# Kernel optimization log

Hardware: AMD Instinct MI355X
Metric: run time of the kernel (lower is better)

Reference implementation:

```python
import jax, jax.numpy as jnp
import numpy as np

B, T, D, H = 4, 1024, 1024, 16
NUM_BUCKETS = 320
MAX_DIST = 800
LN_EPS = 1e-5


def _rel_bucket(T):
    # bidirectional T5-style relative position buckets
    ctx = jnp.arange(T)[:, None]
    mem = jnp.arange(T)[None, :]
    rel = mem - ctx  # (T, T)
    half = NUM_BUCKETS // 2  # 160
    bucket = (rel > 0).astype(jnp.int32) * half
    n = jnp.abs(rel)
    max_exact = half // 2  # 80
    is_small = n < max_exact
    n_f = jnp.maximum(n, 1).astype(jnp.float32)
    large = max_exact + (
        jnp.log(n_f / max_exact) / np.log(MAX_DIST / max_exact) * (half - max_exact)
    ).astype(jnp.int32)
    large = jnp.minimum(large, half - 1)
    return bucket + jnp.where(is_small, n, large)


def setup_inputs() -> dict:
    key = jax.random.key(0)
    ks = jax.random.split(key, 12)
    s = 0.02
    return {
        "x": jax.random.normal(ks[0], (B, T, D), jnp.float32),
        "ln_w": jnp.ones((D,), jnp.float32),
        "ln_b": jnp.zeros((D,), jnp.float32),
        "wq": jax.random.normal(ks[1], (D, D), jnp.float32) * s,
        "bq": jnp.zeros((D,), jnp.float32),
        "wk": jax.random.normal(ks[2], (D, D), jnp.float32) * s,
        "bk": jnp.zeros((D,), jnp.float32),
        "wv": jax.random.normal(ks[3], (D, D), jnp.float32) * s,
        "bv": jnp.zeros((D,), jnp.float32),
        "wo": jax.random.normal(ks[4], (D, D), jnp.float32) * s,
        "bo": jnp.zeros((D,), jnp.float32),
        "rel_emb": jax.random.normal(ks[5], (NUM_BUCKETS, H), jnp.float32) * s,
        "grep_w": jax.random.normal(ks[6], (8, D // H), jnp.float32) * s,
        "grep_b": jnp.zeros((8,), jnp.float32),
        "grep_a": jnp.ones((1, H, 1, 1), jnp.float32),
    }


def reference(x, ln_w, ln_b, wq, bq, wk, bk, wv, bv, wo, bo, rel_emb, grep_w, grep_b, grep_a):
    Bb, Tt, Dd = x.shape
    hd = Dd // H
    scaling = hd ** -0.5
    # pre-norm LayerNorm
    mu = jnp.mean(x, -1, keepdims=True)
    var = jnp.mean((x - mu) ** 2, -1, keepdims=True)
    h = (x - mu) / jnp.sqrt(var + LN_EPS) * ln_w + ln_b
    # projections (q pre-scaled as in fairseq/WavLM)
    q = (h @ wq.T + bq) * scaling
    k = h @ wk.T + bk
    v = h @ wv.T + bv
    q = q.reshape(Bb, Tt, H, hd).transpose(0, 2, 1, 3)  # (B,H,T,hd)
    k = k.reshape(Bb, Tt, H, hd).transpose(0, 2, 1, 3)
    v = v.reshape(Bb, Tt, H, hd).transpose(0, 2, 1, 3)
    # bucketed relative position bias: (H, T, T)
    buckets = _rel_bucket(Tt)
    pos_bias = rel_emb[buckets].transpose(2, 0, 1)
    # gru_rel_pos gating (per batch, head, query position)
    alpha = 32.0
    ql = q * (alpha / scaling)  # undo scaling, multiply by alpha
    g = jax.nn.sigmoid((ql @ grep_w.T + grep_b).reshape(Bb, H, Tt, 2, 4).sum(-1))
    gate_a, gate_b = g[..., 0:1], g[..., 1:2]  # (B,H,T,1)
    gate = gate_a * (gate_b * grep_a - 1.0) + 2.0
    # attention
    scores = jnp.einsum('bhtd,bhsd->bhts', q, k) + gate * pos_bias[None]
    attn = jax.nn.softmax(scores, axis=-1)
    out = jnp.einsum('bhts,bhsd->bhtd', attn, v).transpose(0, 2, 1, 3).reshape(Bb, Tt, Dd)
    # output projection, dropout (identity in eval), residual
    out = out @ wo.T + bo + x
    pos_bias_out = jnp.broadcast_to(pos_bias[None], (Bb, H, Tt, Tt)).reshape(Bb * H, Tt, Tt)
    return out, pos_bias_out
```

## Files before the change

kernel.cpp:

```cpp
#include <hip/hip_runtime.h>

typedef unsigned short u16;
typedef __attribute__((ext_vector_type(8))) short short8;
typedef __attribute__((ext_vector_type(4))) float floatx4;

#define MFMA16(a, b, c) __builtin_amdgcn_mfma_f32_16x16x32_bf16(a, b, c, 0, 0, 0)

__device__ __forceinline__ float bf2f(u16 u) {
  return __uint_as_float(((unsigned int)u) << 16);
}
__device__ __forceinline__ u16 f2bf(float f) {
  unsigned int u = __float_as_uint(f);
  unsigned int r = (u + 0x7fffu + ((u >> 16) & 1u)) >> 16;
  return (u16)r;
}
__device__ __forceinline__ void gl_lds16(const u16* g, u16* lds_wave_base) {
  __builtin_amdgcn_global_load_lds(
      (const __attribute__((address_space(1))) unsigned int*)g,
      (__attribute__((address_space(3))) unsigned int*)lds_wave_base, 16, 0, 0);
}

__global__ __launch_bounds__(256) void ln_kernel(
    const float* __restrict__ x, const float* __restrict__ w, const float* __restrict__ bb,
    u16* __restrict__ hb)
{
  int wid = threadIdx.x >> 6, lane = threadIdx.x & 63;
  int row = blockIdx.x * 4 + wid;
  const float* xr = x + row * 1024 + lane * 16;
  float xs[16];
#pragma unroll
  for (int i = 0; i < 4; i++) {
    float4 v = *(const float4*)(xr + i * 4);
    xs[i * 4 + 0] = v.x; xs[i * 4 + 1] = v.y; xs[i * 4 + 2] = v.z; xs[i * 4 + 3] = v.w;
  }
  float s = 0.f, ss = 0.f;
#pragma unroll
  for (int i = 0; i < 16; i++) { s += xs[i]; ss += xs[i] * xs[i]; }
#pragma unroll
  for (int m = 1; m < 64; m <<= 1) { s += __shfl_xor(s, m, 64); ss += __shfl_xor(ss, m, 64); }
  float mu = s * (1.0f / 1024.0f);
  float var = ss * (1.0f / 1024.0f) - mu * mu;
  float rstd = rsqrtf(var + 1e-5f);
  const float* wr = w + lane * 16;
  const float* br = bb + lane * 16;
  short8 o0, o1;
#pragma unroll
  for (int i = 0; i < 8; i++) {
    o0[i] = (short)f2bf((xs[i] - mu) * rstd * wr[i] + br[i]);
    o1[i] = (short)f2bf((xs[8 + i] - mu) * rstd * wr[8 + i] + br[8 + i]);
  }
  u16* hr = hb + row * 1024 + lane * 16;
  *(short8*)hr = o0;
  *(short8*)(hr + 8) = o1;
}

__global__ __launch_bounds__(256) void convw_kernel(
    const float* __restrict__ wq, const float* __restrict__ wk,
    const float* __restrict__ wv, const float* __restrict__ wo,
    u16* __restrict__ wb)
{
  int idx = (blockIdx.x * 256 + threadIdx.x) * 8;
  int seg = idx >> 20, off = idx & 1048575;
  const float* s = (seg == 0) ? wq : (seg == 1) ? wk : (seg == 2) ? wv : wo;
  float4 f0 = *(const float4*)(s + off);
  float4 f1 = *(const float4*)(s + off + 4);
  short8 o;
  o[0] = (short)f2bf(f0.x); o[1] = (short)f2bf(f0.y);
  o[2] = (short)f2bf(f0.z); o[3] = (short)f2bf(f0.w);
  o[4] = (short)f2bf(f1.x); o[5] = (short)f2bf(f1.y);
  o[6] = (short)f2bf(f1.z); o[7] = (short)f2bf(f1.w);
  *(short8*)&wb[idx] = o;
}

__global__ __launch_bounds__(256) void qkv_kernel(
    const u16* __restrict__ hb, const u16* __restrict__ wb,
    const float* __restrict__ bq, const float* __restrict__ bk, const float* __restrict__ bv,
    u16* __restrict__ qs, u16* __restrict__ kko, u16* __restrict__ vt)
{
  __shared__ u16 As[128 * 32];
  __shared__ u16 Bs[128 * 32];
  int tid = threadIdx.x;
  int wid = tid >> 6, lane = tid & 63;
  int wm = wid >> 1, wn = wid & 1;
  int l15 = lane & 15, quad = lane >> 4;
  int m0 = blockIdx.y * 128;
  int n0g = blockIdx.x * 128;
  int sec = n0g >> 10;
  int n0 = n0g & 1023;
  const u16* W = wb + sec * 1048576;
  const float* bias = (sec == 0) ? bq : ((sec == 1) ? bk : bv);

  floatx4 zero4 = {0.f, 0.f, 0.f, 0.f};
  floatx4 acc[4][4];
#pragma unroll
  for (int i = 0; i < 4; i++)
#pragma unroll
    for (int j = 0; j < 4; j++) acc[i][j] = zero4;

  int lr = tid >> 2;
  int lc = (tid & 3) * 8;
  u16* asw = As + wid * 512;
  u16* bsw = Bs + wid * 512;

  for (int kt = 0; kt < 1024; kt += 32) {
    gl_lds16(&hb[(m0 + lr) * 1024 + kt + lc],      asw);
    gl_lds16(&hb[(m0 + lr + 64) * 1024 + kt + lc], asw + 2048);
    gl_lds16(&W[(n0 + lr) * 1024 + kt + lc],       bsw);
    gl_lds16(&W[(n0 + lr + 64) * 1024 + kt + lc],  bsw + 2048);
    __syncthreads();
    short8 af[4], bf[4];
#pragma unroll
    for (int mi = 0; mi < 4; mi++)
      af[mi] = *(const short8*)&As[(wm * 64 + mi * 16 + l15) * 32 + quad * 8];
#pragma unroll
    for (int ni = 0; ni < 4; ni++)
      bf[ni] = *(const short8*)&Bs[(wn * 64 + ni * 16 + l15) * 32 + quad * 8];
#pragma unroll
    for (int mi = 0; mi < 4; mi++)
#pragma unroll
      for (int ni = 0; ni < 4; ni++)
        acc[mi][ni] = MFMA16(af[mi], bf[ni], acc[mi][ni]);
    __syncthreads();
  }

  int bidx = m0 >> 10;
#pragma unroll
  for (int mi = 0; mi < 4; mi++) {
#pragma unroll
    for (int ni = 0; ni < 4; ni++) {
#pragma unroll
      for (int r = 0; r < 4; r++) {
        int row = m0 + wm * 64 + mi * 16 + quad * 4 + r;
        int t = row & 1023;
        int c = n0 + wn * 64 + ni * 16 + l15;
        float val = acc[mi][ni][r] + bias[c];
        int hh = c >> 6, hp = c & 63;
        if (sec == 0) {
          val *= 0.125f;
          qs[((bidx * 16 + hh) * 1024 + t) * 64 + hp] = f2bf(val);
        } else if (sec == 1) {
          kko[((bidx * 16 + hh) * 1024 + t) * 64 + hp] = f2bf(val);
        } else {
          vt[((bidx * 16 + hh) * 64 + hp) * 1024 + t] = f2bf(val);
        }
      }
    }
  }
}

__device__ __forceinline__ int rel_bucket(int t, int s) {
  int rel = s - t;
  int bucket = (rel > 0) ? 160 : 0;
  int n = (rel < 0) ? -rel : rel;
  if (n < 80) return bucket + n;
  float a = logf((float)n / 80.0f);
  float c = a / (float)2.302585092994046;
  float v = c * 80.0f;
  int large = 80 + (int)v;
  if (large > 159) large = 159;
  return bucket + large;
}

__global__ __launch_bounds__(256) void bias0_kernel(
    const float* __restrict__ rel_emb, float* __restrict__ out1,
    u16* __restrict__ bh16, int nb4)
{
  int tid = blockIdx.x * 256 + threadIdx.x;
  int t = tid >> 7;
  int s0 = (tid & 127) * 8;
  int bkt[8];
#pragma unroll
  for (int j = 0; j < 8; j++) bkt[j] = rel_bucket(t, s0 + j) * 16;
  int base_ts = t * 1024 + s0;
#pragma unroll
  for (int hh = 0; hh < 16; hh++) {
    float4 v0, v1;
    v0.x = rel_emb[bkt[0] + hh]; v0.y = rel_emb[bkt[1] + hh];
    v0.z = rel_emb[bkt[2] + hh]; v0.w = rel_emb[bkt[3] + hh];
    v1.x = rel_emb[bkt[4] + hh]; v1.y = rel_emb[bkt[5] + hh];
    v1.z = rel_emb[bkt[6] + hh]; v1.w = rel_emb[bkt[7] + hh];
    float* p = out1 + hh * 1048576 + base_ts;
    *(float4*)p = v0;
    *(float4*)(p + 4) = v1;
    if (nb4) {
      *(float4*)(p + 16777216) = v0; *(float4*)(p + 16777216 + 4) = v1;
      *(float4*)(p + 33554432) = v0; *(float4*)(p + 33554432 + 4) = v1;
      *(float4*)(p + 50331648) = v0; *(float4*)(p + 50331648 + 4) = v1;
    }
    short8 o;
    o[0] = (short)f2bf(v0.x); o[1] = (short)f2bf(v0.y);
    o[2] = (short)f2bf(v0.z); o[3] = (short)f2bf(v0.w);
    o[4] = (short)f2bf(v1.x); o[5] = (short)f2bf(v1.y);
    o[6] = (short)f2bf(v1.z); o[7] = (short)f2bf(v1.w);
    *(short8*)(bh16 + hh * 1048576 + base_ts) = o;
  }
}

__global__ __launch_bounds__(256) void bias_copy_kernel(float* __restrict__ out1)
{
  int idx = blockIdx.x * 256 + threadIdx.x;
  float4 v = *(const float4*)&out1[idx * 4];
  *(float4*)&out1[16777216 + idx * 4] = v;
  *(float4*)&out1[33554432 + idx * 4] = v;
  *(float4*)&out1[50331648 + idx * 4] = v;
}

__global__ __launch_bounds__(256) void attn_kernel(
    const u16* __restrict__ qs, const u16* __restrict__ kko, const u16* __restrict__ vt,
    const float* __restrict__ gw, const float* __restrict__ gb, const float* __restrict__ ga,
    const u16* __restrict__ bh16, u16* __restrict__ ao)
{
  __shared__ __align__(16) u16 Pb[4][16 * 64];
  int wid = threadIdx.x >> 6, lane = threadIdx.x & 63;
  int l15 = lane & 15, quad = lane >> 4;
  int bh = blockIdx.x;
  int b = bh >> 4, h = bh & 15;
  int q0 = blockIdx.y * 64 + wid * 16;
  const u16* Q = qs + bh * 65536;
  const u16* K = kko + bh * 65536;
  const u16* V = vt + bh * 65536;
  const u16* Bi = bh16 + h * 1048576;
  u16* pb = &Pb[wid][0];

  const u16* qrow = Q + (q0 + l15) * 64;
  float e[8];
#pragma unroll
  for (int i = 0; i < 8; i++) e[i] = gb[i];
  for (int j = 0; j < 64; j++) {
    float ql = bf2f(qrow[j]) * 256.0f;
#pragma unroll
    for (int i = 0; i < 8; i++) e[i] += ql * gw[i * 64 + j];
  }
  float u0 = e[0] + e[1] + e[2] + e[3];
  float u1 = e[4] + e[5] + e[6] + e[7];
  float sa = 1.0f / (1.0f + __expf(-u0));
  float sb = 1.0f / (1.0f + __expf(-u1));
  float gv = sa * (sb * ga[h] - 1.0f) + 2.0f;

  short8 qf0 = *(const short8*)&Q[(q0 + l15) * 64 + quad * 8];
  short8 qf1 = *(const short8*)&Q[(q0 + l15) * 64 + quad * 8 + 32];
  float gt[4], mrun[4], lrun[4];
#pragma unroll
  for (int r = 0; r < 4; r++) {
    gt[r] = __shfl(gv, quad * 4 + r, 64);
    mrun[r] = -1e30f;
    lrun[r] = 0.f;
  }
  floatx4 zero4 = {0.f, 0.f, 0.f, 0.f};
  floatx4 accO[4];
#pragma unroll
  for (int ni = 0; ni < 4; ni++) accO[ni] = zero4;

  for (int s0 = 0; s0 < 1024; s0 += 64) {
    floatx4 sc[4];
#pragma unroll
    for (int j = 0; j < 4; j++) sc[j] = zero4;
    short8 kf;
#pragma unroll
    for (int j = 0; j < 4; j++) {
      kf = *(const short8*)&K[(s0 + j * 16 + l15) * 64 + quad * 8];
      sc[j] = MFMA16(qf0, kf, sc[j]);
      kf = *(const short8*)&K[(s0 + j * 16 + l15) * 64 + quad * 8 + 32];
      sc[j] = MFMA16(qf1, kf, sc[j]);
    }

#pragma unroll
    for (int r = 0; r < 4; r++) {
      int t = q0 + quad * 4 + r;
      float v[4];
#pragma unroll
      for (int j = 0; j < 4; j++)
        v[j] = sc[j][r] + gt[r] * bf2f(Bi[t * 1024 + s0 + j * 16 + l15]);
      float mt = fmaxf(fmaxf(v[0], v[1]), fmaxf(v[2], v[3]));
#pragma unroll
      for (int m = 1; m < 16; m <<= 1) mt = fmaxf(mt, __shfl_xor(mt, m, 64));
      float mnew = fmaxf(mrun[r], mt);
      float alpha = __expf(fmaxf(mrun[r] - mnew, -80.0f));
      float p[4], ps = 0.f;
#pragma unroll
      for (int j = 0; j < 4; j++) { p[j] = __expf(v[j] - mnew); ps += p[j]; }
#pragma unroll
      for (int m = 1; m < 16; m <<= 1) ps += __shfl_xor(ps, m, 64);
      lrun[r] = lrun[r] * alpha + ps;
      mrun[r] = mnew;
#pragma unroll
      for (int ni = 0; ni < 4; ni++) accO[ni][r] *= alpha;
#pragma unroll
      for (int j = 0; j < 4; j++)
        pb[(quad * 4 + r) * 64 + j * 16 + l15] = f2bf(p[j]);
    }
    __syncthreads();
    short8 pf0 = *(const short8*)&pb[l15 * 64 + quad * 8];
    short8 pf1 = *(const short8*)&pb[l15 * 64 + 32 + quad * 8];
#pragma unroll
    for (int ni = 0; ni < 4; ni++) {
      short8 vf = *(const short8*)&V[(ni * 16 + l15) * 1024 + s0 + quad * 8];
      accO[ni] = MFMA16(pf0, vf, accO[ni]);
      vf = *(const short8*)&V[(ni * 16 + l15) * 1024 + s0 + 32 + quad * 8];
      accO[ni] = MFMA16(pf1, vf, accO[ni]);
    }
  }
#pragma unroll
  for (int ni = 0; ni < 4; ni++) {
#pragma unroll
    for (int r = 0; r < 4; r++) {
      int t = q0 + quad * 4 + r;
      float val = accO[ni][r] / lrun[r];
      ao[(b * 1024 + t) * 1024 + h * 64 + ni * 16 + l15] = f2bf(val);
    }
  }
}

__global__ __launch_bounds__(256) void oproj_kernel(
    const u16* __restrict__ ao, const u16* __restrict__ wob, const float* __restrict__ bo,
    const float* __restrict__ x, float* __restrict__ out)
{
  __shared__ u16 As[128 * 32];
  __shared__ u16 Bs[128 * 32];
  int tid = threadIdx.x;
  int wid = tid >> 6, lane = tid & 63;
  int wm = wid >> 1, wn = wid & 1;
  int l15 = lane & 15, quad = lane >> 4;
  int m0 = blockIdx.y * 128;
  int n0 = blockIdx.x * 128;

  floatx4 zero4 = {0.f, 0.f, 0.f, 0.f};
  floatx4 acc[4][4];
#pragma unroll
  for (int i = 0; i < 4; i++)
#pragma unroll
    for (int j = 0; j < 4; j++) acc[i][j] = zero4;

  int lr = tid >> 2;
  int lc = (tid & 3) * 8;
  u16* asw = As + wid * 512;
  u16* bsw = Bs + wid * 512;

  for (int kt = 0; kt < 1024; kt += 32) {
    gl_lds16(&ao[(m0 + lr) * 1024 + kt + lc],       asw);
    gl_lds16(&ao[(m0 + lr + 64) * 1024 + kt + lc],  asw + 2048);
    gl_lds16(&wob[(n0 + lr) * 1024 + kt + lc],      bsw);
    gl_lds16(&wob[(n0 + lr + 64) * 1024 + kt + lc], bsw + 2048);
    __syncthreads();
    short8 af[4], bf[4];
#pragma unroll
    for (int mi = 0; mi < 4; mi++)
      af[mi] = *(const short8*)&As[(wm * 64 + mi * 16 + l15) * 32 + quad * 8];
#pragma unroll
    for (int ni = 0; ni < 4; ni++)
      bf[ni] = *(const short8*)&Bs[(wn * 64 + ni * 16 + l15) * 32 + quad * 8];
#pragma unroll
    for (int mi = 0; mi < 4; mi++)
#pragma unroll
      for (int ni = 0; ni < 4; ni++)
        acc[mi][ni] = MFMA16(af[mi], bf[ni], acc[mi][ni]);
    __syncthreads();
  }

#pragma unroll
  for (int mi = 0; mi < 4; mi++) {
#pragma unroll
    for (int ni = 0; ni < 4; ni++) {
#pragma unroll
      for (int r = 0; r < 4; r++) {
        int row = m0 + wm * 64 + mi * 16 + quad * 4 + r;
        int c = n0 + wn * 64 + ni * 16 + l15;
        out[row * 1024 + c] = acc[mi][ni][r] + bo[c] + x[row * 1024 + c];
      }
    }
  }
}

extern "C" void kernel_launch(void* const* d_in, const int* in_sizes, int n_in,
                              void* d_out, int out_size, void* d_ws, size_t ws_size,
                              hipStream_t stream) {
  const float* x    = (const float*)d_in[0];
  const float* ln_w = (const float*)d_in[1];
  const float* ln_b = (const float*)d_in[2];
  const float* wq   = (const float*)d_in[3];
  const float* bq   = (const float*)d_in[4];
  const float* wk   = (const float*)d_in[5];
  const float* bk   = (const float*)d_in[6];
  const float* wv   = (const float*)d_in[7];
  const float* bv   = (const float*)d_in[8];
  const float* wo   = (const float*)d_in[9];
  const float* bo   = (const float*)d_in[10];
  const float* rel  = (const float*)d_in[11];
  const float* gw   = (const float*)d_in[12];
  const float* gb   = (const float*)d_in[13];
  const float* ga   = (const float*)d_in[14];

  float* out0  = (float*)d_out;
  float* out1f = out0 + 4194304;

  int big_ws = (ws_size >= (size_t)(96u << 20)) ? 1 : 0;
  char* sb = big_ws ? (char*)d_ws : (char*)(out1f + 16777216);
  u16* hbb = (u16*)(sb);
  u16* wbb = (u16*)(sb + (8u << 20));
  u16* qsb = (u16*)(sb + (16u << 20));
  u16* kkb = (u16*)(sb + (24u << 20));
  u16* vtb = (u16*)(sb + (32u << 20));
  u16* aob = (u16*)(sb + (40u << 20));
  u16* bhb = (u16*)(sb + (48u << 20));

  ln_kernel<<<1024, 256, 0, stream>>>(x, ln_w, ln_b, hbb);
  convw_kernel<<<2048, 256, 0, stream>>>(wq, wk, wv, wo, wbb);
  qkv_kernel<<<dim3(24, 32), 256, 0, stream>>>(hbb, wbb, bq, bk, bv, qsb, kkb, vtb);
  bias0_kernel<<<512, 256, 0, stream>>>(rel, out1f, bhb, big_ws);
  attn_kernel<<<dim3(64, 16), 256, 0, stream>>>(qsb, kkb, vtb, gw, gb, ga, bhb, aob);
  oproj_kernel<<<dim3(8, 32), 256, 0, stream>>>(aob, wbb + 3145728, bo, x, out0);
  if (!big_ws)
    bias_copy_kernel<<<16384, 256, 0, stream>>>(out1f);
}
```

Measured before the change: 594.6 us.

## Defer softmax row-sum reduction, pad P LDS tile, replace barrier with waitcnt

In the attention kernel, each lane now keeps a per-lane partial row sum and does the cross-lane shuffle reduction once at the end, instead of reducing every 64-key tile. The block-wide __syncthreads before reading the P tile becomes an lgkmcnt wait, since each wave only reads its own LDS slice. The P tile rows are padded from 64 to 68 elements to cut LDS bank conflicts, and the bias loads are hoisted ahead of the QK MFMAs to overlap their latency. The risks are relying on intra-wave LDS ordering without a barrier and the padded layout forcing 8-byte LDS reads instead of 16-byte ones.

Measured after the change: 552.2 us. 1.08x faster.

```diff
diff --git a/kernel.cpp b/kernel.cpp
--- a/kernel.cpp
+++ b/kernel.cpp
@@ -2,6 +2,7 @@
 
 typedef unsigned short u16;
 typedef __attribute__((ext_vector_type(8))) short short8;
+typedef __attribute__((ext_vector_type(4))) short short4v;
 typedef __attribute__((ext_vector_type(4))) float floatx4;
 
 #define MFMA16(a, b, c) __builtin_amdgcn_mfma_f32_16x16x32_bf16(a, b, c, 0, 0, 0)
@@ -210,7 +211,7 @@
     const float* __restrict__ gw, const float* __restrict__ gb, const float* __restrict__ ga,
     const u16* __restrict__ bh16, u16* __restrict__ ao)
 {
-  __shared__ __align__(16) u16 Pb[4][16 * 64];
+  __shared__ __align__(16) u16 Pb[4][16 * 68];
   int wid = threadIdx.x >> 6, lane = threadIdx.x & 63;
   int l15 = lane & 15, quad = lane >> 4;
   int bh = blockIdx.x;
@@ -239,12 +240,12 @@
 
   short8 qf0 = *(const short8*)&Q[(q0 + l15) * 64 + quad * 8];
   short8 qf1 = *(const short8*)&Q[(q0 + l15) * 64 + quad * 8 + 32];
-  float gt[4], mrun[4], lrun[4];
+  float gt[4], mrun[4], lsum[4];
 #pragma unroll
   for (int r = 0; r < 4; r++) {
     gt[r] = __shfl(gv, quad * 4 + r, 64);
     mrun[r] = -1e30f;
-    lrun[r] = 0.f;
+    lsum[r] = 0.f;
   }
   floatx4 zero4 = {0.f, 0.f, 0.f, 0.f};
   floatx4 accO[4];
@@ -252,13 +253,20 @@
   for (int ni = 0; ni < 4; ni++) accO[ni] = zero4;
 
   for (int s0 = 0; s0 < 1024; s0 += 64) {
+    float bi[4][4];
+#pragma unroll
+    for (int r = 0; r < 4; r++) {
+      int t = q0 + quad * 4 + r;
+#pragma unroll
+      for (int j = 0; j < 4; j++)
+        bi[r][j] = bf2f(Bi[t * 1024 + s0 + j * 16 + l15]);
+    }
     floatx4 sc[4];
 #pragma unroll
     for (int j = 0; j < 4; j++) sc[j] = zero4;
-    short8 kf;
 #pragma unroll
     for (int j = 0; j < 4; j++) {
-      kf = *(const short8*)&K[(s0 + j * 16 + l15) * 64 + quad * 8];
+      short8 kf = *(const short8*)&K[(s0 + j * 16 + l15) * 64 + quad * 8];
       sc[j] = MFMA16(qf0, kf, sc[j]);
       kf = *(const short8*)&K[(s0 + j * 16 + l15) * 64 + quad * 8 + 32];
       sc[j] = MFMA16(qf1, kf, sc[j]);
@@ -266,32 +274,33 @@
 
 #pragma unroll
     for (int r = 0; r < 4; r++) {
-      int t = q0 + quad * 4 + r;
       float v[4];
 #pragma unroll
-      for (int j = 0; j < 4; j++)
-        v[j] = sc[j][r] + gt[r] * bf2f(Bi[t * 1024 + s0 + j * 16 + l15]);
+      for (int j = 0; j < 4; j++) v[j] = sc[j][r] + gt[r] * bi[r][j];
       float mt = fmaxf(fmaxf(v[0], v[1]), fmaxf(v[2], v[3]));
 #pragma unroll
       for (int m = 1; m < 16; m <<= 1) mt = fmaxf(mt, __shfl_xor(mt, m, 64));
       float mnew = fmaxf(mrun[r], mt);
       float alpha = __expf(fmaxf(mrun[r] - mnew, -80.0f));
-      float p[4], ps = 0.f;
-#pragma unroll
-      for (int j = 0; j < 4; j++) { p[j] = __expf(v[j] - mnew); ps += p[j]; }
-#pragma unroll
-      for (int m = 1; m < 16; m <<= 1) ps += __shfl_xor(ps, m, 64);
-      lrun[r] = lrun[r] * alpha + ps;
+      float p[4];
+#pragma unroll
+      for (int j = 0; j < 4; j++) p[j] = __expf(v[j] - mnew);
+      lsum[r] = lsum[r] * alpha + (p[0] + p[1]) + (p[2] + p[3]);
       mrun[r] = mnew;
 #pragma unroll
       for (int ni = 0; ni < 4; ni++) accO[ni][r] *= alpha;
 #pragma unroll
       for (int j = 0; j < 4; j++)
-        pb[(quad * 4 + r) * 64 + j * 16 + l15] = f2bf(p[j]);
-    }
-    __syncthreads();
-    short8 pf0 = *(const short8*)&pb[l15 * 64 + quad * 8];
-    short8 pf1 = *(const short8*)&pb[l15 * 64 + 32 + quad * 8];
+        pb[(quad * 4 + r) * 68 + j * 16 + l15] = f2bf(p[j]);
+    }
+    __asm__ __volatile__("s_waitcnt lgkmcnt(0)" ::: "memory");
+    short4v a0 = *(const short4v*)&pb[l15 * 68 + quad * 8];
+    short4v a1 = *(const short4v*)&pb[l15 * 68 + quad * 8 + 4];
+    short4v a2 = *(const short4v*)&pb[l15 * 68 + 32 + quad * 8];
+    short4v a3 = *(const short4v*)&pb[l15 * 68 + 32 + quad * 8 + 4];
+    short8 pf0, pf1;
+#pragma unroll
+    for (int i = 0; i < 4; i++) { pf0[i] = a0[i]; pf0[4 + i] = a1[i]; pf1[i] = a2[i]; pf1[4 + i] = a3[i]; }
 #pragma unroll
     for (int ni = 0; ni < 4; ni++) {
       short8 vf = *(const short8*)&V[(ni * 16 + l15) * 1024 + s0 + quad * 8];
@@ -300,13 +309,20 @@
       accO[ni] = MFMA16(pf1, vf, accO[ni]);
     }
   }
+  float linv[4];
+#pragma unroll
+  for (int r = 0; r < 4; r++) {
+    float ls = lsum[r];
+#pragma unroll
+    for (int m = 1; m < 16; m <<= 1) ls += __shfl_xor(ls, m, 64);
+    linv[r] = 1.0f / ls;
+  }
 #pragma unroll
   for (int ni = 0; ni < 4; ni++) {
 #pragma unroll
     for (int r = 0; r < 4; r++) {
       int t = q0 + quad * 4 + r;
-      float val = accO[ni][r] / lrun[r];
-      ao[(b * 1024 + t) * 1024 + h * 64 + ni * 16 + l15] = f2bf(val);
+      ao[(b * 1024 + t) * 1024 + h * 64 + ni * 16 + l15] = f2bf(accO[ni][r] * linv[r]);
     }
   }
 }
```

## Transpose attention score tiles so each lane owns one query column

Applied to the files above, without the earlier changes.

Swaps the MFMA operands so that score and output tiles are computed transposed. Each lane now holds one query's scores, which lets the softmax max and sum be reduced mostly in registers with two cross-quad shuffles instead of per-row 16-lane shuffle trees. The bf16 bias table is written transposed so the attention kernel's bias reads become contiguous across lanes. It also pads the P buffer in LDS, replaces `__syncthreads` with a wave-local `lgkmcnt` wait, adds an occupancy hint to the launch bounds, and stages the final output through LDS to restore row-major stores. In exchange it adds extra LDS round trips and relies on the P buffer being private to each wave.

Result: faster. 567.7 us (-4.5%).

```diff
diff --git a/kernel.cpp b/kernel.cpp
--- a/kernel.cpp
+++ b/kernel.cpp
@@ -2,6 +2,7 @@
 
 typedef unsigned short u16;
 typedef __attribute__((ext_vector_type(8))) short short8;
+typedef __attribute__((ext_vector_type(4))) short short4v;
 typedef __attribute__((ext_vector_type(4))) float floatx4;
 
 #define MFMA16(a, b, c) __builtin_amdgcn_mfma_f32_16x16x32_bf16(a, b, c, 0, 0, 0)
@@ -168,9 +169,12 @@
   int tid = blockIdx.x * 256 + threadIdx.x;
   int t = tid >> 7;
   int s0 = (tid & 127) * 8;
-  int bkt[8];
-#pragma unroll
-  for (int j = 0; j < 8; j++) bkt[j] = rel_bucket(t, s0 + j) * 16;
+  int bkt[8], bktT[8];
+#pragma unroll
+  for (int j = 0; j < 8; j++) {
+    bkt[j]  = rel_bucket(t, s0 + j) * 16;
+    bktT[j] = rel_bucket(s0 + j, t) * 16;
+  }
   int base_ts = t * 1024 + s0;
 #pragma unroll
   for (int hh = 0; hh < 16; hh++) {
@@ -188,10 +192,8 @@
       *(float4*)(p + 50331648) = v0; *(float4*)(p + 50331648 + 4) = v1;
     }
     short8 o;
-    o[0] = (short)f2bf(v0.x); o[1] = (short)f2bf(v0.y);
-    o[2] = (short)f2bf(v0.z); o[3] = (short)f2bf(v0.w);
-    o[4] = (short)f2bf(v1.x); o[5] = (short)f2bf(v1.y);
-    o[6] = (short)f2bf(v1.z); o[7] = (short)f2bf(v1.w);
+#pragma unroll
+    for (int j = 0; j < 8; j++) o[j] = (short)f2bf(rel_emb[bktT[j] + hh]);
     *(short8*)(bh16 + hh * 1048576 + base_ts) = o;
   }
 }
@@ -205,12 +207,12 @@
   *(float4*)&out1[50331648 + idx * 4] = v;
 }
 
-__global__ __launch_bounds__(256) void attn_kernel(
+__global__ __launch_bounds__(256, 4) void attn_kernel(
     const u16* __restrict__ qs, const u16* __restrict__ kko, const u16* __restrict__ vt,
     const float* __restrict__ gw, const float* __restrict__ gb, const float* __restrict__ ga,
     const u16* __restrict__ bh16, u16* __restrict__ ao)
 {
-  __shared__ __align__(16) u16 Pb[4][16 * 64];
+  __shared__ __align__(16) u16 Pb[4][16 * 72];
   int wid = threadIdx.x >> 6, lane = threadIdx.x & 63;
   int l15 = lane & 15, quad = lane >> 4;
   int bh = blockIdx.x;
@@ -219,7 +221,7 @@
   const u16* Q = qs + bh * 65536;
   const u16* K = kko + bh * 65536;
   const u16* V = vt + bh * 65536;
-  const u16* Bi = bh16 + h * 1048576;
+  const u16* BiT = bh16 + h * 1048576;
   u16* pb = &Pb[wid][0];
 
   const u16* qrow = Q + (q0 + l15) * 64;
@@ -235,17 +237,11 @@
   float u1 = e[4] + e[5] + e[6] + e[7];
   float sa = 1.0f / (1.0f + __expf(-u0));
   float sb = 1.0f / (1.0f + __expf(-u1));
-  float gv = sa * (sb * ga[h] - 1.0f) + 2.0f;
+  float gt = sa * (sb * ga[h] - 1.0f) + 2.0f;
 
   short8 qf0 = *(const short8*)&Q[(q0 + l15) * 64 + quad * 8];
   short8 qf1 = *(const short8*)&Q[(q0 + l15) * 64 + quad * 8 + 32];
-  float gt[4], mrun[4], lrun[4];
-#pragma unroll
-  for (int r = 0; r < 4; r++) {
-    gt[r] = __shfl(gv, quad * 4 + r, 64);
-    mrun[r] = -1e30f;
-    lrun[r] = 0.f;
-  }
+  float mrun = -1e30f, lsum = 0.f;
   floatx4 zero4 = {0.f, 0.f, 0.f, 0.f};
   floatx4 accO[4];
 #pragma unroll
@@ -254,59 +250,70 @@
   for (int s0 = 0; s0 < 1024; s0 += 64) {
     floatx4 sc[4];
 #pragma unroll
-    for (int j = 0; j < 4; j++) sc[j] = zero4;
-    short8 kf;
-#pragma unroll
-    for (int j = 0; j < 4; j++) {
-      kf = *(const short8*)&K[(s0 + j * 16 + l15) * 64 + quad * 8];
-      sc[j] = MFMA16(qf0, kf, sc[j]);
-      kf = *(const short8*)&K[(s0 + j * 16 + l15) * 64 + quad * 8 + 32];
-      sc[j] = MFMA16(qf1, kf, sc[j]);
-    }
-
-#pragma unroll
-    for (int r = 0; r < 4; r++) {
-      int t = q0 + quad * 4 + r;
-      float v[4];
-#pragma unroll
-      for (int j = 0; j < 4; j++)
-        v[j] = sc[j][r] + gt[r] * bf2f(Bi[t * 1024 + s0 + j * 16 + l15]);
-      float mt = fmaxf(fmaxf(v[0], v[1]), fmaxf(v[2], v[3]));
-#pragma unroll
-      for (int m = 1; m < 16; m <<= 1) mt = fmaxf(mt, __shfl_xor(mt, m, 64));
-      float mnew = fmaxf(mrun[r], mt);
-      float alpha = __expf(fmaxf(mrun[r] - mnew, -80.0f));
-      float p[4], ps = 0.f;
-#pragma unroll
-      for (int j = 0; j < 4; j++) { p[j] = __expf(v[j] - mnew); ps += p[j]; }
-#pragma unroll
-      for (int m = 1; m < 16; m <<= 1) ps += __shfl_xor(ps, m, 64);
-      lrun[r] = lrun[r] * alpha + ps;
-      mrun[r] = mnew;
-#pragma unroll
-      for (int ni = 0; ni < 4; ni++) accO[ni][r] *= alpha;
-#pragma unroll
-      for (int j = 0; j < 4; j++)
-        pb[(quad * 4 + r) * 64 + j * 16 + l15] = f2bf(p[j]);
-    }
-    __syncthreads();
-    short8 pf0 = *(const short8*)&pb[l15 * 64 + quad * 8];
-    short8 pf1 = *(const short8*)&pb[l15 * 64 + 32 + quad * 8];
+    for (int tile = 0; tile < 4; tile++) {
+      short8 kf = *(const short8*)&K[(s0 + tile * 16 + l15) * 64 + quad * 8];
+      sc[tile] = MFMA16(kf, qf0, zero4);
+      kf = *(const short8*)&K[(s0 + tile * 16 + l15) * 64 + quad * 8 + 32];
+      sc[tile] = MFMA16(kf, qf1, sc[tile]);
+    }
+    float v[16];
+    float mt = -1e30f;
+#pragma unroll
+    for (int tile = 0; tile < 4; tile++)
+#pragma unroll
+      for (int r = 0; r < 4; r++) {
+        int s = s0 + tile * 16 + quad * 4 + r;
+        float val = sc[tile][r] + gt * bf2f(BiT[s * 1024 + q0 + l15]);
+        v[tile * 4 + r] = val;
+        mt = fmaxf(mt, val);
+      }
+    mt = fmaxf(mt, __shfl_xor(mt, 16, 64));
+    mt = fmaxf(mt, __shfl_xor(mt, 32, 64));
+    float mnew = fmaxf(mrun, mt);
+    float alpha = __expf(fmaxf(mrun - mnew, -80.0f));
+    mrun = mnew;
+    float psum = 0.f;
+#pragma unroll
+    for (int i = 0; i < 16; i++) { v[i] = __expf(v[i] - mnew); psum += v[i]; }
+    lsum = lsum * alpha + psum;
+#pragma unroll
+    for (int ni = 0; ni < 4; ni++) accO[ni] *= alpha;
+#pragma unroll
+    for (int tile = 0; tile < 4; tile++) {
+      short4v o;
+#pragma unroll
+      for (int r = 0; r < 4; r++) o[r] = (short)f2bf(v[tile * 4 + r]);
+      *(short4v*)&pb[l15 * 72 + tile * 16 + quad * 4] = o;
+    }
+    __asm__ __volatile__("s_waitcnt lgkmcnt(0)" ::: "memory");
+    short8 pf0 = *(const short8*)&pb[l15 * 72 + quad * 8];
+    short8 pf1 = *(const short8*)&pb[l15 * 72 + 32 + quad * 8];
 #pragma unroll
     for (int ni = 0; ni < 4; ni++) {
       short8 vf = *(const short8*)&V[(ni * 16 + l15) * 1024 + s0 + quad * 8];
-      accO[ni] = MFMA16(pf0, vf, accO[ni]);
+      accO[ni] = MFMA16(vf, pf0, accO[ni]);
       vf = *(const short8*)&V[(ni * 16 + l15) * 1024 + s0 + 32 + quad * 8];
-      accO[ni] = MFMA16(pf1, vf, accO[ni]);
-    }
-  }
+      accO[ni] = MFMA16(vf, pf1, accO[ni]);
+    }
+  }
+  lsum += __shfl_xor(lsum, 16, 64);
+  lsum += __shfl_xor(lsum, 32, 64);
+  float linv = 1.0f / lsum;
 #pragma unroll
   for (int ni = 0; ni < 4; ni++) {
-#pragma unroll
-    for (int r = 0; r < 4; r++) {
-      int t = q0 + quad * 4 + r;
-      float val = accO[ni][r] / lrun[r];
-      ao[(b * 1024 + t) * 1024 + h * 64 + ni * 16 + l15] = f2bf(val);
+    short4v o;
+#pragma unroll
+    for (int r = 0; r < 4; r++) o[r] = (short)f2bf(accO[ni][r] * linv);
+    *(short4v*)&pb[l15 * 72 + ni * 16 + quad * 4] = o;
+  }
+  __asm__ __volatile__("s_waitcnt lgkmcnt(0)" ::: "memory");
+#pragma unroll
+  for (int r = 0; r < 4; r++) {
+    int t = q0 + quad * 4 + r;
+#pragma unroll
+    for (int ni = 0; ni < 4; ni++) {
+      u16 val = pb[(quad * 4 + r) * 72 + ni * 16 + l15];
+      ao[(b * 1024 + t) * 1024 + h * 64 + ni * 16 + l15] = val;
     }
   }
 }
```
